# Kernel optimization log

Measured on AMD Instinct MI355X. Metric: run time of the kernel, lower is better.

## Reference

```python
import jax, jax.numpy as jnp
from jax import lax
import numpy as np

EPS = 1e-3  # Keras BatchNormalization default epsilon

def cond_conv(x, experts, rw, rb):
    # x: [B,H,W,Cin]; experts: [E,kh,kw,Cin,Cout]
    pooled = jnp.mean(x, axis=(1, 2))                       # [B,Cin]
    route = jax.nn.sigmoid(pooled @ rw + rb)                # [B,E]
    kernels = jnp.einsum('be,ehwio->bhwio', route, experts) # per-example kernel
    def conv1(xi, ki):
        return lax.conv_general_dilated(
            xi[None], ki, window_strides=(1, 1), padding='SAME',
            dimension_numbers=('NHWC', 'HWIO', 'NHWC'))[0]
    return jax.vmap(conv1)(x, kernels)

def bn_inf(x, gamma, beta, mean, var):
    inv = gamma * lax.rsqrt(var + EPS)
    return x * inv + (beta - mean * inv)

def maxpool2(x):
    return lax.reduce_window(x, -jnp.inf, lax.max,
                             (1, 2, 2, 1), (1, 2, 2, 1), 'SAME')

def se_block(x, w1, w2):
    s = jnp.mean(x, axis=(1, 2))          # [B,C]
    s = jax.nn.relu(s @ w1)
    s = jax.nn.sigmoid(s @ w2)
    return x * s[:, None, None, :]

def setup_inputs() -> dict:
    key = jax.random.key(0)
    ks = jax.random.split(key, 12)
    d = {
        'x': jax.random.normal(ks[0], (64, 128, 128, 6), jnp.float32),
        'experts1': jax.random.normal(ks[1], (3, 3, 3, 6, 32), jnp.float32) * 0.1,
        'route1_w': jax.random.normal(ks[2], (6, 3), jnp.float32) * 0.1,
        'route1_b': jnp.zeros((3,), jnp.float32),
        'bn1_gamma': jnp.ones((32,), jnp.float32), 'bn1_beta': jnp.zeros((32,), jnp.float32),
        'bn1_mean': jnp.zeros((32,), jnp.float32), 'bn1_var': jnp.ones((32,), jnp.float32),
        'se1_w1': jax.random.normal(ks[3], (32, 2), jnp.float32) * 0.1,
        'se1_w2': jax.random.normal(ks[4], (2, 32), jnp.float32) * 0.1,
        'experts2': jax.random.normal(ks[5], (3, 3, 3, 32, 64), jnp.float32) * 0.05,
        'route2_w': jax.random.normal(ks[6], (32, 3), jnp.float32) * 0.1,
        'route2_b': jnp.zeros((3,), jnp.float32),
        'bn2_gamma': jnp.ones((64,), jnp.float32), 'bn2_beta': jnp.zeros((64,), jnp.float32),
        'bn2_mean': jnp.zeros((64,), jnp.float32), 'bn2_var': jnp.ones((64,), jnp.float32),
        'se2_w1': jax.random.normal(ks[7], (64, 4), jnp.float32) * 0.1,
        'se2_w2': jax.random.normal(ks[8], (4, 64), jnp.float32) * 0.1,
        'experts3': jax.random.normal(ks[9], (3, 3, 3, 64, 128), jnp.float32) * 0.05,
        'route3_w': jax.random.normal(ks[10], (64, 3), jnp.float32) * 0.1,
        'route3_b': jnp.zeros((3,), jnp.float32),
        'bn3_gamma': jnp.ones((128,), jnp.float32), 'bn3_beta': jnp.zeros((128,), jnp.float32),
        'bn3_mean': jnp.zeros((128,), jnp.float32), 'bn3_var': jnp.ones((128,), jnp.float32),
    }
    return d

def reference(x, experts1, route1_w, route1_b, bn1_gamma, bn1_beta, bn1_mean, bn1_var,
              se1_w1, se1_w2, experts2, route2_w, route2_b, bn2_gamma, bn2_beta,
              bn2_mean, bn2_var, se2_w1, se2_w2, experts3, route3_w, route3_b,
              bn3_gamma, bn3_beta, bn3_mean, bn3_var):
    h = cond_conv(x, experts1, route1_w, route1_b)
    h = jax.nn.relu(bn_inf(h, bn1_gamma, bn1_beta, bn1_mean, bn1_var))
    h = maxpool2(h)                       # [B,64,64,32]
    h = se_block(h, se1_w1, se1_w2)
    h = cond_conv(h, experts2, route2_w, route2_b)
    h = jax.nn.relu(bn_inf(h, bn2_gamma, bn2_beta, bn2_mean, bn2_var))
    h = maxpool2(h)                       # [B,32,32,64]
    h = se_block(h, se2_w1, se2_w2)
    h = cond_conv(h, experts3, route3_w, route3_b)
    h = bn_inf(h, bn3_gamma, bn3_beta, bn3_mean, bn3_var)
    return jnp.mean(h, axis=(1, 2))       # [B,128]
```

## Files before the change

kernel.cpp:

```cpp
#include <hip/hip_runtime.h>

#define EPSBN 1e-3f

typedef unsigned short ushort_t;
typedef __attribute__((ext_vector_type(8))) short bf8;
typedef __attribute__((ext_vector_type(4))) float f4;

__device__ __forceinline__ float sigmoidf_(float z) {
  return 1.0f / (1.0f + expf(-z));
}

__device__ __forceinline__ ushort_t f2bf(float x) {
  union { float f; unsigned u; } v; v.f = x;
  unsigned r = (v.u + 0x7fffu + ((v.u >> 16) & 1u)) >> 16;
  return (ushort_t)r;
}

__global__ void k_mean_x(const float* __restrict__ x, float* __restrict__ part) {
  const int b = blockIdx.x >> 2;
  const int q = blockIdx.x & 3;
  const int tid = threadIdx.x;
  float acc[6] = {0.f, 0.f, 0.f, 0.f, 0.f, 0.f};
  const float* xb = x + (size_t)b * (128 * 128 * 6);
  for (int i = 0; i < 16; ++i) {
    const int p = q * 4096 + i * 256 + tid;
    const float* px = xb + (size_t)p * 6;
#pragma unroll
    for (int c = 0; c < 6; ++c) acc[c] += px[c];
  }
#pragma unroll
  for (int c = 0; c < 6; ++c)
    for (int off = 32; off > 0; off >>= 1) acc[c] += __shfl_down(acc[c], off, 64);
  __shared__ float red[4][6];
  const int lane = tid & 63, w = tid >> 6;
  if (lane == 0) {
#pragma unroll
    for (int c = 0; c < 6; ++c) red[w][c] = acc[c];
  }
  __syncthreads();
  if (tid < 6) {
    part[blockIdx.x * 6 + tid] = red[0][tid] + red[1][tid] + red[2][tid] + red[3][tid];
  }
}

__global__ void k_buildk1(const float* __restrict__ part,
                          const float* __restrict__ experts1,
                          const float* __restrict__ rw, const float* __restrict__ rb,
                          const float* __restrict__ gamma, const float* __restrict__ var,
                          ushort_t* __restrict__ k1b) {
  const int b = blockIdx.x;
  const int tid = threadIdx.x;
  __shared__ float route[3];
  if (tid < 3) {
    float z = rb[tid];
    for (int c = 0; c < 6; ++c) {
      const float s = part[(b * 4 + 0) * 6 + c] + part[(b * 4 + 1) * 6 + c] +
                      part[(b * 4 + 2) * 6 + c] + part[(b * 4 + 3) * 6 + c];
      z += (s * (1.0f / 16384.0f)) * rw[c * 3 + tid];
    }
    route[tid] = sigmoidf_(z);
  }
  __syncthreads();
  const float r0 = route[0], r1 = route[1], r2 = route[2];
  for (int s = tid; s < 3072; s += 256) {
    const int j = s & 7;
    const int lane = (s >> 3) & 63;
    const int nt = (s >> 9) & 1;
    const int ky = s >> 10;
    const int lx = lane & 15, lg = lane >> 4;
    const int co = nt * 16 + lx;
    float val = 0.f;
    if (lg < 3 && j < 6) {
      const int idx = ((ky * 3 + lg) * 6 + j) * 32 + co;
      const float v = r0 * experts1[idx] + r1 * experts1[1728 + idx] + r2 * experts1[3456 + idx];
      val = v * gamma[co] * rsqrtf(var[co] + EPSBN);
    }
    k1b[(size_t)b * 3072 + s] = f2bf(val);
  }
}

__global__ __launch_bounds__(256)
void k_conv1(const float* __restrict__ x, const ushort_t* __restrict__ k1b,
             const float* __restrict__ gamma, const float* __restrict__ beta,
             const float* __restrict__ bnmean, const float* __restrict__ bnvar,
             ushort_t* __restrict__ p1b, float* __restrict__ part_m1) {
  const int bid = blockIdx.x;
  const int b = bid >> 3;
  const int tyi = (bid >> 1) & 3;
  const int txi = bid & 1;
  __shared__ __align__(16) ushort_t patch[34 * 68 * 8];
  __shared__ float mred[4][32];
  const int tid = threadIdx.x;
  const float* xb = x + (size_t)b * (128 * 128 * 6);

  for (int v = tid; v < 34 * 68; v += 256) {
    const int ry = v / 68, p = v - ry * 68;
    const int gy = tyi * 32 - 1 + ry, gx = txi * 64 - 1 + p;
    uint4 u = make_uint4(0u, 0u, 0u, 0u);
    if (((unsigned)gy < 128u) && ((unsigned)gx < 128u)) {
      const float* s = xb + ((size_t)(gy * 128 + gx)) * 6;
      const float2 a0 = *(const float2*)s;
      const float2 a1 = *(const float2*)(s + 2);
      const float2 a2 = *(const float2*)(s + 4);
      u.x = (unsigned)f2bf(a0.x) | ((unsigned)f2bf(a0.y) << 16);
      u.y = (unsigned)f2bf(a1.x) | ((unsigned)f2bf(a1.y) << 16);
      u.z = (unsigned)f2bf(a2.x) | ((unsigned)f2bf(a2.y) << 16);
      u.w = 0u;
    }
    *(uint4*)(patch + (size_t)v * 8) = u;
  }

  const int w = tid >> 6;
  const int lane = tid & 63;
  const int lx = lane & 15, lg = lane >> 4;

  bf8 Bf[3][2];
#pragma unroll
  for (int ky = 0; ky < 3; ++ky)
#pragma unroll
    for (int nt = 0; nt < 2; ++nt)
      Bf[ky][nt] = *(const bf8*)(k1b + (size_t)b * 3072 + ((size_t)((ky * 2 + nt) * 64 + lane)) * 8);

  const int co0 = lx, co1 = 16 + lx;
  const float inv0 = gamma[co0] * rsqrtf(bnvar[co0] + EPSBN);
  const float bias0 = beta[co0] - bnmean[co0] * inv0;
  const float inv1 = gamma[co1] * rsqrtf(bnvar[co1] + EPSBN);
  const float bias1 = beta[co1] - bnmean[co1] * inv1;

  __syncthreads();

  float msum0 = 0.f, msum1 = 0.f;

#pragma unroll
  for (int rp = 0; rp < 4; ++rp) {
    const int y0 = w * 8 + rp * 2;
    const int prow = tyi * 16 + w * 4 + rp;
#pragma unroll
    for (int xt = 0; xt < 4; ++xt) {
      bf8 Af[4];
#pragma unroll
      for (int ri = 0; ri < 4; ++ri)
        Af[ri] = *(const bf8*)(patch + ((size_t)(y0 + ri) * 68 + xt * 16 + lx + lg) * 8);
      f4 acc0[2], acc1[2];
#pragma unroll
      for (int nt = 0; nt < 2; ++nt) {
        acc0[nt] = (f4){0.f, 0.f, 0.f, 0.f};
        acc1[nt] = (f4){0.f, 0.f, 0.f, 0.f};
      }
#pragma unroll
      for (int ky = 0; ky < 3; ++ky) {
#pragma unroll
        for (int nt = 0; nt < 2; ++nt) {
          acc0[nt] = __builtin_amdgcn_mfma_f32_16x16x32_bf16(Af[ky], Bf[ky][nt], acc0[nt], 0, 0, 0);
          acc1[nt] = __builtin_amdgcn_mfma_f32_16x16x32_bf16(Af[ky + 1], Bf[ky][nt], acc1[nt], 0, 0, 0);
        }
      }
#pragma unroll
      for (int nt = 0; nt < 2; ++nt) {
        const float inv = nt ? inv1 : inv0;
        const float bias = nt ? bias1 : bias0;
        const int co = nt * 16 + lx;
#pragma unroll
        for (int q = 0; q < 2; ++q) {
          const float m0 = fmaxf(acc0[nt][2 * q] + bias, 0.f);
          const float m1 = fmaxf(acc0[nt][2 * q + 1] + bias, 0.f);
          const float m2 = fmaxf(acc1[nt][2 * q] + bias, 0.f);
          const float m3 = fmaxf(acc1[nt][2 * q + 1] + bias, 0.f);
          const float mx = fmaxf(fmaxf(m0, m1), fmaxf(m2, m3));
          if (nt) msum1 += mx; else msum0 += mx;
          const int pcol = txi * 32 + xt * 8 + lg * 2 + q;
          p1b[(((size_t)b * 64 + prow) * 64 + pcol) * 32 + co] = f2bf(mx);
        }
      }
    }
  }

  msum0 += __shfl_xor(msum0, 16, 64);
  msum0 += __shfl_xor(msum0, 32, 64);
  msum1 += __shfl_xor(msum1, 16, 64);
  msum1 += __shfl_xor(msum1, 32, 64);
  if (lg == 0) {
    mred[w][lx] = msum0;
    mred[w][16 + lx] = msum1;
  }
  __syncthreads();
  if (tid < 32) {
    part_m1[(size_t)bid * 32 + tid] =
        mred[0][tid] + mred[1][tid] + mred[2][tid] + mred[3][tid];
  }
}

__global__ void k_buildk2(const float* __restrict__ part_m1,
                          const float* __restrict__ experts2,
                          const float* __restrict__ rw, const float* __restrict__ rb,
                          const float* __restrict__ w1, const float* __restrict__ w2,
                          const float* __restrict__ gamma, const float* __restrict__ var,
                          ushort_t* __restrict__ k2pb) {
  const int b = blockIdx.x, tid = threadIdx.x;
  __shared__ float m1[32], h[2], s1[32], route[3];
  if (tid < 32) {
    float s = 0.f;
#pragma unroll
    for (int k = 0; k < 8; ++k) s += part_m1[(size_t)(b * 8 + k) * 32 + tid];
    m1[tid] = s * (1.0f / 4096.0f);
  }
  __syncthreads();
  if (tid < 2) {
    float z = 0.f;
    for (int c = 0; c < 32; ++c) z += m1[c] * w1[c * 2 + tid];
    h[tid] = fmaxf(z, 0.f);
  }
  __syncthreads();
  if (tid < 32) s1[tid] = sigmoidf_(h[0] * w2[tid] + h[1] * w2[32 + tid]);
  __syncthreads();
  if (tid < 3) {
    float z = rb[tid];
    for (int c = 0; c < 32; ++c) z += m1[c] * s1[c] * rw[c * 3 + tid];
    route[tid] = sigmoidf_(z);
  }
  __syncthreads();
  const float r0 = route[0], r1 = route[1], r2 = route[2];
  for (int t = tid; t < 18432; t += 256) {
    const int co = t & 63;
    const int ci = (t >> 6) & 31;
    const int tap = t >> 11;
    const float inv = gamma[co] * rsqrtf(var[co] + EPSBN);
    const float v = r0 * experts2[t] + r1 * experts2[18432 + t] + r2 * experts2[2 * 18432 + t];
    k2pb[(size_t)b * 18432 + ((size_t)tap * 64 + co) * 32 + ci] = f2bf(v * s1[ci] * inv);
  }
}

__global__ __launch_bounds__(256)
void k_conv2(const ushort_t* __restrict__ p1b, const ushort_t* __restrict__ k2pb,
             const float* __restrict__ gamma, const float* __restrict__ beta,
             const float* __restrict__ bnmean, const float* __restrict__ bnvar,
             float* __restrict__ part_s3) {
  const int bi = blockIdx.x;
  const int b = bi >> 5;
  const int tile = (bi >> 1) & 15;
  const int cog = bi & 1;
  const int ty = tile >> 2, tx = tile & 3;
  __shared__ __align__(16) short smem[24480];
  __shared__ float sred[4][2][16][9];
  short* As = smem;
  short* Bs = smem + 12960;
  const int tid = threadIdx.x;

  const ushort_t* pb = p1b + (size_t)b * 131072;
  for (int v = tid; v < 1296; v += 256) {
    const int cell = v >> 2, part = v & 3;
    const int ly = cell / 18, lx2 = cell - ly * 18;
    const int gy = ty * 16 - 1 + ly, gx = tx * 16 - 1 + lx2;
    uint4 d = make_uint4(0u, 0u, 0u, 0u);
    if (((unsigned)gy < 64u) && ((unsigned)gx < 64u))
      d = *(const uint4*)(pb + (((size_t)gy << 6) + gx) * 32 + part * 8);
    *(uint4*)(As + (ly * 18 + lx2) * 40 + part * 8) = d;
  }
  for (int v = tid; v < 1152; v += 256) {
    const int r = v >> 2, part = v & 3;
    const int t = r >> 5, n = r & 31;
    const uint4 d = *(const uint4*)(k2pb + (size_t)b * 18432 +
                                    ((size_t)(t * 64 + cog * 32 + n)) * 32 + part * 8);
    *(uint4*)(Bs + r * 40 + part * 8) = d;
  }
  __syncthreads();

  const int w = tid >> 6;
  const int lane = tid & 63;
  const int lx = lane & 15, lg = lane >> 4;

  f4 acc[4][2];
#pragma unroll
  for (int mt = 0; mt < 4; ++mt)
#pragma unroll
    for (int nt = 0; nt < 2; ++nt)
      acc[mt][nt] = (f4){0.f, 0.f, 0.f, 0.f};

#pragma unroll
  for (int t = 0; t < 9; ++t) {
    const int ky = t / 3, kx = t - 3 * (t / 3);
    bf8 Bf0 = *(const bf8*)(Bs + ((t << 5) + lx) * 40 + (lg << 3));
    bf8 Bf1 = *(const bf8*)(Bs + ((t << 5) + 16 + lx) * 40 + (lg << 3));
#pragma unroll
    for (int mt = 0; mt < 4; ++mt) {
      const int y = 4 * w + mt + ky;
      const bf8 Af = *(const bf8*)(As + (y * 18 + lx + kx) * 40 + (lg << 3));
      acc[mt][0] = __builtin_amdgcn_mfma_f32_16x16x32_bf16(Af, Bf0, acc[mt][0], 0, 0, 0);
      acc[mt][1] = __builtin_amdgcn_mfma_f32_16x16x32_bf16(Af, Bf1, acc[mt][1], 0, 0, 0);
    }
  }

  float s3[2][9];
#pragma unroll
  for (int nt = 0; nt < 2; ++nt)
#pragma unroll
    for (int t = 0; t < 9; ++t) s3[nt][t] = 0.f;

#pragma unroll
  for (int half = 0; half < 2; ++half) {
    const int prow = ty * 8 + 2 * w + half;
    const bool rok0 = (prow < 31), rok2 = (prow > 0);
#pragma unroll
    for (int q = 0; q < 2; ++q) {
      const int pcol = tx * 8 + 2 * lg + q;
      const bool cok0 = (pcol < 31), cok2 = (pcol > 0);
      const bool rok[3] = {rok0, true, rok2};
      const bool cok[3] = {cok0, true, cok2};
#pragma unroll
      for (int nt = 0; nt < 2; ++nt) {
        const int co = cog * 32 + nt * 16 + lx;
        const float inv = gamma[co] * rsqrtf(bnvar[co] + EPSBN);
        const float bias = beta[co] - bnmean[co] * inv;
        const float m0 = fmaxf(acc[2 * half][nt][2 * q] + bias, 0.f);
        const float m1 = fmaxf(acc[2 * half][nt][2 * q + 1] + bias, 0.f);
        const float m2 = fmaxf(acc[2 * half + 1][nt][2 * q] + bias, 0.f);
        const float m3 = fmaxf(acc[2 * half + 1][nt][2 * q + 1] + bias, 0.f);
        const float mx = fmaxf(fmaxf(m0, m1), fmaxf(m2, m3));
#pragma unroll
        for (int ky = 0; ky < 3; ++ky)
#pragma unroll
          for (int kx = 0; kx < 3; ++kx)
            if (rok[ky] && cok[kx]) s3[nt][ky * 3 + kx] += mx;
      }
    }
  }

#pragma unroll
  for (int nt = 0; nt < 2; ++nt)
#pragma unroll
    for (int t = 0; t < 9; ++t) {
      float v = s3[nt][t];
      v += __shfl_xor(v, 16, 64);
      v += __shfl_xor(v, 32, 64);
      s3[nt][t] = v;
    }
  __syncthreads();
  if (lg == 0) {
#pragma unroll
    for (int nt = 0; nt < 2; ++nt)
#pragma unroll
      for (int t = 0; t < 9; ++t) sred[w][nt][lx][t] = s3[nt][t];
  }
  __syncthreads();
  for (int v = tid; v < 288; v += 256) {
    const int tap = v >> 5;
    const int colocal = v & 31;
    const int nt = colocal >> 4, lxx = colocal & 15;
    part_s3[(size_t)bi * 288 + v] =
        sred[0][nt][lxx][tap] + sred[1][nt][lxx][tap] +
        sred[2][nt][lxx][tap] + sred[3][nt][lxx][tap];
  }
}

__global__ __launch_bounds__(512)
void k_final(const float* __restrict__ part_s3, const float* __restrict__ experts3,
             const float* __restrict__ rw, const float* __restrict__ rb,
             const float* __restrict__ w1, const float* __restrict__ w2,
             const float* __restrict__ gamma, const float* __restrict__ beta,
             const float* __restrict__ bnmean, const float* __restrict__ bnvar,
             float* __restrict__ out) {
  const int b = blockIdx.x;
  const int tid = threadIdx.x;
  __shared__ float S_loc[9][64], Sp[9][64], m2[64], h[4], s2[64], route[3], redf[4][128];

  for (int v = tid; v < 576; v += 512) {
    const int tap = v >> 6, ci = v & 63;
    const int cg = ci >> 5, colocal = ci & 31;
    float s = 0.f;
#pragma unroll
    for (int tile = 0; tile < 16; ++tile)
      s += part_s3[(size_t)((b * 16 + tile) * 2 + cg) * 288 + tap * 32 + colocal];
    S_loc[tap][ci] = s;
  }
  __syncthreads();
  if (tid < 64) m2[tid] = S_loc[4][tid] * (1.0f / 1024.0f);
  __syncthreads();
  if (tid < 4) {
    float z = 0.f;
    for (int c = 0; c < 64; ++c) z += m2[c] * w1[c * 4 + tid];
    h[tid] = fmaxf(z, 0.f);
  }
  __syncthreads();
  if (tid < 64) {
    float z = 0.f;
#pragma unroll
    for (int j = 0; j < 4; ++j) z += h[j] * w2[j * 64 + tid];
    s2[tid] = sigmoidf_(z);
  }
  __syncthreads();
  if (tid < 3) {
    float z = rb[tid];
    for (int c = 0; c < 64; ++c) z += m2[c] * s2[c] * rw[c * 3 + tid];
    route[tid] = sigmoidf_(z);
  }
  __syncthreads();
  for (int v = tid; v < 576; v += 512) {
    const int tap = v >> 6, ci = v & 63;
    Sp[tap][ci] = S_loc[tap][ci] * s2[ci];
  }
  __syncthreads();

  const int co = tid & 127;
  const int quarter = tid >> 7;
  const int tap_lo = (quarter == 0) ? 0 : (2 * quarter + 1);
  const int tap_hi = tap_lo + ((quarter == 0) ? 3 : 2);
  float acc = 0.f;
#pragma unroll
  for (int e = 0; e < 3; ++e) {
    float m = 0.f;
    for (int tap = tap_lo; tap < tap_hi; ++tap) {
      const float* E = experts3 + ((size_t)(e * 9 + tap) * 64) * 128 + co;
#pragma unroll 16
      for (int ci = 0; ci < 64; ++ci) m = fmaf(E[(size_t)ci * 128], Sp[tap][ci], m);
    }
    acc += route[e] * m;
  }
  redf[quarter][co] = acc;
  __syncthreads();
  if (tid < 128) {
    const float total = redf[0][tid] + redf[1][tid] + redf[2][tid] + redf[3][tid];
    const float inv = gamma[tid] * rsqrtf(bnvar[tid] + EPSBN);
    out[(size_t)b * 128 + tid] = total * (1.0f / 1024.0f) * inv + (beta[tid] - bnmean[tid] * inv);
  }
}

extern "C" void kernel_launch(void* const* d_in, const int* in_sizes, int n_in,
                              void* d_out, int out_size, void* d_ws, size_t ws_size,
                              hipStream_t stream) {
  const float* x        = (const float*)d_in[0];
  const float* experts1 = (const float*)d_in[1];
  const float* rw1      = (const float*)d_in[2];
  const float* rb1      = (const float*)d_in[3];
  const float* g1  = (const float*)d_in[4];
  const float* be1 = (const float*)d_in[5];
  const float* mu1 = (const float*)d_in[6];
  const float* va1 = (const float*)d_in[7];
  const float* sw1a = (const float*)d_in[8];
  const float* sw1b = (const float*)d_in[9];
  const float* experts2 = (const float*)d_in[10];
  const float* rw2 = (const float*)d_in[11];
  const float* rb2 = (const float*)d_in[12];
  const float* g2  = (const float*)d_in[13];
  const float* be2 = (const float*)d_in[14];
  const float* mu2 = (const float*)d_in[15];
  const float* va2 = (const float*)d_in[16];
  const float* sw2a = (const float*)d_in[17];
  const float* sw2b = (const float*)d_in[18];
  const float* experts3 = (const float*)d_in[19];
  const float* rw3 = (const float*)d_in[20];
  const float* rb3 = (const float*)d_in[21];
  const float* g3  = (const float*)d_in[22];
  const float* be3 = (const float*)d_in[23];
  const float* mu3 = (const float*)d_in[24];
  const float* va3 = (const float*)d_in[25];
  float* out = (float*)d_out;
  float* ws = (float*)d_ws;

  float* meanx_part = ws;
  float* part_m1    = ws + 1536;
  ushort_t* k1b     = (ushort_t*)(ws + 17920);
  ushort_t* k2pb    = (ushort_t*)(ws + 116224);
  float* part_s3    = ws + 706048;
  ushort_t* p1b     = (ushort_t*)(ws + 1295872);

  hipLaunchKernelGGL(k_mean_x, dim3(256), dim3(256), 0, stream, x, meanx_part);
  hipLaunchKernelGGL(k_buildk1, dim3(64), dim3(256), 0, stream,
                     meanx_part, experts1, rw1, rb1, g1, va1, k1b);
  hipLaunchKernelGGL(k_conv1, dim3(512), dim3(256), 0, stream,
                     x, k1b, g1, be1, mu1, va1, p1b, part_m1);
  hipLaunchKernelGGL(k_buildk2, dim3(64), dim3(256), 0, stream,
                     part_m1, experts2, rw2, rb2, sw1a, sw1b, g2, va2, k2pb);
  hipLaunchKernelGGL(k_conv2, dim3(2048), dim3(256), 0, stream,
                     p1b, k2pb, g2, be2, mu2, va2, part_s3);
  hipLaunchKernelGGL(k_final, dim3(64), dim3(512), 0, stream,
                     part_s3, experts3, rw3, rb3, sw2a, sw2b, g3, be3, mu3, va3, out);
}
```

Before: 207.3 us.

## Fuse conv1 kernel build into conv1, vectorize mean, reuse A fragments, restructure border sums

The k_buildk1 kernel is removed and conv1 now computes the routing and builds its bf16 weight fragments in registers, which saves a launch and a global round trip. k_mean_x switches to float4 contiguous loads. Both conv kernels load A fragments once and reuse them across output rows or taps, which cuts LDS reads. k_buildk2 is spread over three times as many blocks. conv2 now records the total plus border row, column and corner sums, and the final kernel rebuilds the per-tap sums from these by inclusion-exclusion. That reduces the conditional accumulation and hoists the BN constants out of the loop, at the cost of more registers and redundant weight construction in every conv1 block.

```diff
diff --git a/kernel.cpp b/kernel.cpp
--- a/kernel.cpp
+++ b/kernel.cpp
@@ -21,12 +21,17 @@
   const int q = blockIdx.x & 3;
   const int tid = threadIdx.x;
   float acc[6] = {0.f, 0.f, 0.f, 0.f, 0.f, 0.f};
-  const float* xb = x + (size_t)b * (128 * 128 * 6);
-  for (int i = 0; i < 16; ++i) {
-    const int p = q * 4096 + i * 256 + tid;
-    const float* px = xb + (size_t)p * 6;
-#pragma unroll
-    for (int c = 0; c < 6; ++c) acc[c] += px[c];
+  const float* xb = x + (size_t)b * 98304 + (size_t)q * 24576;
+  for (int p = 0; p < 4; ++p) {
+    const float* base = xb + (size_t)p * 6144 + (size_t)tid * 24;
+#pragma unroll
+    for (int k = 0; k < 6; ++k) {
+      const float4 v = *(const float4*)(base + k * 4);
+      acc[(4 * k + 0) % 6] += v.x;
+      acc[(4 * k + 1) % 6] += v.y;
+      acc[(4 * k + 2) % 6] += v.z;
+      acc[(4 * k + 3) % 6] += v.w;
+    }
   }
 #pragma unroll
   for (int c = 0; c < 6; ++c)
@@ -43,44 +48,10 @@
   }
 }
 
-__global__ void k_buildk1(const float* __restrict__ part,
-                          const float* __restrict__ experts1,
-                          const float* __restrict__ rw, const float* __restrict__ rb,
-                          const float* __restrict__ gamma, const float* __restrict__ var,
-                          ushort_t* __restrict__ k1b) {
-  const int b = blockIdx.x;
-  const int tid = threadIdx.x;
-  __shared__ float route[3];
-  if (tid < 3) {
-    float z = rb[tid];
-    for (int c = 0; c < 6; ++c) {
-      const float s = part[(b * 4 + 0) * 6 + c] + part[(b * 4 + 1) * 6 + c] +
-                      part[(b * 4 + 2) * 6 + c] + part[(b * 4 + 3) * 6 + c];
-      z += (s * (1.0f / 16384.0f)) * rw[c * 3 + tid];
-    }
-    route[tid] = sigmoidf_(z);
-  }
-  __syncthreads();
-  const float r0 = route[0], r1 = route[1], r2 = route[2];
-  for (int s = tid; s < 3072; s += 256) {
-    const int j = s & 7;
-    const int lane = (s >> 3) & 63;
-    const int nt = (s >> 9) & 1;
-    const int ky = s >> 10;
-    const int lx = lane & 15, lg = lane >> 4;
-    const int co = nt * 16 + lx;
-    float val = 0.f;
-    if (lg < 3 && j < 6) {
-      const int idx = ((ky * 3 + lg) * 6 + j) * 32 + co;
-      const float v = r0 * experts1[idx] + r1 * experts1[1728 + idx] + r2 * experts1[3456 + idx];
-      val = v * gamma[co] * rsqrtf(var[co] + EPSBN);
-    }
-    k1b[(size_t)b * 3072 + s] = f2bf(val);
-  }
-}
-
 __global__ __launch_bounds__(256)
-void k_conv1(const float* __restrict__ x, const ushort_t* __restrict__ k1b,
+void k_conv1(const float* __restrict__ x, const float* __restrict__ meanx_part,
+             const float* __restrict__ experts1,
+             const float* __restrict__ rw, const float* __restrict__ rbias,
              const float* __restrict__ gamma, const float* __restrict__ beta,
              const float* __restrict__ bnmean, const float* __restrict__ bnvar,
              ushort_t* __restrict__ p1b, float* __restrict__ part_m1) {
@@ -89,9 +60,20 @@
   const int tyi = (bid >> 1) & 3;
   const int txi = bid & 1;
   __shared__ __align__(16) ushort_t patch[34 * 68 * 8];
+  __shared__ float route_s[3];
   __shared__ float mred[4][32];
   const int tid = threadIdx.x;
   const float* xb = x + (size_t)b * (128 * 128 * 6);
+
+  if (tid < 3) {
+    float z = rbias[tid];
+    for (int c = 0; c < 6; ++c) {
+      const float s = meanx_part[(b * 4 + 0) * 6 + c] + meanx_part[(b * 4 + 1) * 6 + c] +
+                      meanx_part[(b * 4 + 2) * 6 + c] + meanx_part[(b * 4 + 3) * 6 + c];
+      z += (s * (1.0f / 16384.0f)) * rw[c * 3 + tid];
+    }
+    route_s[tid] = sigmoidf_(z);
+  }
 
   for (int v = tid; v < 34 * 68; v += 256) {
     const int ry = v / 68, p = v - ry * 68;
@@ -109,38 +91,50 @@
     }
     *(uint4*)(patch + (size_t)v * 8) = u;
   }
+  __syncthreads();
 
   const int w = tid >> 6;
   const int lane = tid & 63;
   const int lx = lane & 15, lg = lane >> 4;
 
-  bf8 Bf[3][2];
-#pragma unroll
-  for (int ky = 0; ky < 3; ++ky)
-#pragma unroll
-    for (int nt = 0; nt < 2; ++nt)
-      Bf[ky][nt] = *(const bf8*)(k1b + (size_t)b * 3072 + ((size_t)((ky * 2 + nt) * 64 + lane)) * 8);
-
+  const float r0 = route_s[0], r1 = route_s[1], r2 = route_s[2];
   const int co0 = lx, co1 = 16 + lx;
   const float inv0 = gamma[co0] * rsqrtf(bnvar[co0] + EPSBN);
   const float bias0 = beta[co0] - bnmean[co0] * inv0;
   const float inv1 = gamma[co1] * rsqrtf(bnvar[co1] + EPSBN);
   const float bias1 = beta[co1] - bnmean[co1] * inv1;
 
-  __syncthreads();
+  bf8 Bf[3][2];
+#pragma unroll
+  for (int ky = 0; ky < 3; ++ky) {
+#pragma unroll
+    for (int nt = 0; nt < 2; ++nt) {
+      const int co = nt * 16 + lx;
+      const float inv = nt ? inv1 : inv0;
+#pragma unroll
+      for (int j = 0; j < 8; ++j) {
+        float val = 0.f;
+        if (j < 6 && lg < 3) {
+          const int idx = ((ky * 3 + lg) * 6 + j) * 32 + co;
+          val = (r0 * experts1[idx] + r1 * experts1[1728 + idx] +
+                 r2 * experts1[3456 + idx]) * inv;
+        }
+        Bf[ky][nt][j] = (short)f2bf(val);
+      }
+    }
+  }
 
   float msum0 = 0.f, msum1 = 0.f;
 
 #pragma unroll
-  for (int rp = 0; rp < 4; ++rp) {
-    const int y0 = w * 8 + rp * 2;
-    const int prow = tyi * 16 + w * 4 + rp;
-#pragma unroll
-    for (int xt = 0; xt < 4; ++xt) {
-      bf8 Af[4];
-#pragma unroll
-      for (int ri = 0; ri < 4; ++ri)
-        Af[ri] = *(const bf8*)(patch + ((size_t)(y0 + ri) * 68 + xt * 16 + lx + lg) * 8);
+  for (int xt = 0; xt < 4; ++xt) {
+    bf8 Af[10];
+#pragma unroll
+    for (int r = 0; r < 10; ++r)
+      Af[r] = *(const bf8*)(patch + ((size_t)(w * 8 + r) * 68 + xt * 16 + lx + lg) * 8);
+#pragma unroll
+    for (int rp = 0; rp < 4; ++rp) {
+      const int prow = tyi * 16 + w * 4 + rp;
       f4 acc0[2], acc1[2];
 #pragma unroll
       for (int nt = 0; nt < 2; ++nt) {
@@ -151,13 +145,12 @@
       for (int ky = 0; ky < 3; ++ky) {
 #pragma unroll
         for (int nt = 0; nt < 2; ++nt) {
-          acc0[nt] = __builtin_amdgcn_mfma_f32_16x16x32_bf16(Af[ky], Bf[ky][nt], acc0[nt], 0, 0, 0);
-          acc1[nt] = __builtin_amdgcn_mfma_f32_16x16x32_bf16(Af[ky + 1], Bf[ky][nt], acc1[nt], 0, 0, 0);
+          acc0[nt] = __builtin_amdgcn_mfma_f32_16x16x32_bf16(Af[rp * 2 + ky], Bf[ky][nt], acc0[nt], 0, 0, 0);
+          acc1[nt] = __builtin_amdgcn_mfma_f32_16x16x32_bf16(Af[rp * 2 + ky + 1], Bf[ky][nt], acc1[nt], 0, 0, 0);
         }
       }
 #pragma unroll
       for (int nt = 0; nt < 2; ++nt) {
-        const float inv = nt ? inv1 : inv0;
         const float bias = nt ? bias1 : bias0;
         const int co = nt * 16 + lx;
 #pragma unroll
@@ -196,7 +189,9 @@
                           const float* __restrict__ w1, const float* __restrict__ w2,
                           const float* __restrict__ gamma, const float* __restrict__ var,
                           ushort_t* __restrict__ k2pb) {
-  const int b = blockIdx.x, tid = threadIdx.x;
+  const int b = blockIdx.x / 3;
+  const int seg = blockIdx.x - b * 3;
+  const int tid = threadIdx.x;
   __shared__ float m1[32], h[2], s1[32], route[3];
   if (tid < 32) {
     float s = 0.f;
@@ -220,7 +215,8 @@
   }
   __syncthreads();
   const float r0 = route[0], r1 = route[1], r2 = route[2];
-  for (int t = tid; t < 18432; t += 256) {
+  const int t_lo = seg * 6144, t_hi = t_lo + 6144;
+  for (int t = t_lo + tid; t < t_hi; t += 256) {
     const int co = t & 63;
     const int ci = (t >> 6) & 31;
     const int tap = t >> 11;
@@ -241,7 +237,6 @@
   const int cog = bi & 1;
   const int ty = tile >> 2, tx = tile & 3;
   __shared__ __align__(16) short smem[24480];
-  __shared__ float sred[4][2][16][9];
   short* As = smem;
   short* Bs = smem + 12960;
   const int tid = threadIdx.x;
@@ -277,50 +272,61 @@
       acc[mt][nt] = (f4){0.f, 0.f, 0.f, 0.f};
 
 #pragma unroll
-  for (int t = 0; t < 9; ++t) {
-    const int ky = t / 3, kx = t - 3 * (t / 3);
-    bf8 Bf0 = *(const bf8*)(Bs + ((t << 5) + lx) * 40 + (lg << 3));
-    bf8 Bf1 = *(const bf8*)(Bs + ((t << 5) + 16 + lx) * 40 + (lg << 3));
-#pragma unroll
-    for (int mt = 0; mt < 4; ++mt) {
-      const int y = 4 * w + mt + ky;
-      const bf8 Af = *(const bf8*)(As + (y * 18 + lx + kx) * 40 + (lg << 3));
-      acc[mt][0] = __builtin_amdgcn_mfma_f32_16x16x32_bf16(Af, Bf0, acc[mt][0], 0, 0, 0);
-      acc[mt][1] = __builtin_amdgcn_mfma_f32_16x16x32_bf16(Af, Bf1, acc[mt][1], 0, 0, 0);
-    }
-  }
-
-  float s3[2][9];
+  for (int kx = 0; kx < 3; ++kx) {
+    bf8 Af[6];
+#pragma unroll
+    for (int r = 0; r < 6; ++r)
+      Af[r] = *(const bf8*)(As + ((4 * w + r) * 18 + lx + kx) * 40 + (lg << 3));
+#pragma unroll
+    for (int ky = 0; ky < 3; ++ky) {
+      const int t = ky * 3 + kx;
+      const bf8 Bf0 = *(const bf8*)(Bs + ((t << 5) + lx) * 40 + (lg << 3));
+      const bf8 Bf1 = *(const bf8*)(Bs + ((t << 5) + 16 + lx) * 40 + (lg << 3));
+#pragma unroll
+      for (int mt = 0; mt < 4; ++mt) {
+        acc[mt][0] = __builtin_amdgcn_mfma_f32_16x16x32_bf16(Af[ky + mt], Bf0, acc[mt][0], 0, 0, 0);
+        acc[mt][1] = __builtin_amdgcn_mfma_f32_16x16x32_bf16(Af[ky + mt], Bf1, acc[mt][1], 0, 0, 0);
+      }
+    }
+  }
+
+  float inv[2], bias[2];
+#pragma unroll
+  for (int nt = 0; nt < 2; ++nt) {
+    const int co = cog * 32 + nt * 16 + lx;
+    inv[nt] = gamma[co] * rsqrtf(bnvar[co] + EPSBN);
+    bias[nt] = beta[co] - bnmean[co] * inv[nt];
+  }
+  float agg[2][9];
 #pragma unroll
   for (int nt = 0; nt < 2; ++nt)
 #pragma unroll
-    for (int t = 0; t < 9; ++t) s3[nt][t] = 0.f;
+    for (int a = 0; a < 9; ++a) agg[nt][a] = 0.f;
 
 #pragma unroll
   for (int half = 0; half < 2; ++half) {
     const int prow = ty * 8 + 2 * w + half;
-    const bool rok0 = (prow < 31), rok2 = (prow > 0);
+    const bool rT = (prow == 0), rB = (prow == 31);
 #pragma unroll
     for (int q = 0; q < 2; ++q) {
       const int pcol = tx * 8 + 2 * lg + q;
-      const bool cok0 = (pcol < 31), cok2 = (pcol > 0);
-      const bool rok[3] = {rok0, true, rok2};
-      const bool cok[3] = {cok0, true, cok2};
+      const bool cL = (pcol == 0), cR = (pcol == 31);
 #pragma unroll
       for (int nt = 0; nt < 2; ++nt) {
-        const int co = cog * 32 + nt * 16 + lx;
-        const float inv = gamma[co] * rsqrtf(bnvar[co] + EPSBN);
-        const float bias = beta[co] - bnmean[co] * inv;
-        const float m0 = fmaxf(acc[2 * half][nt][2 * q] + bias, 0.f);
-        const float m1 = fmaxf(acc[2 * half][nt][2 * q + 1] + bias, 0.f);
-        const float m2 = fmaxf(acc[2 * half + 1][nt][2 * q] + bias, 0.f);
-        const float m3 = fmaxf(acc[2 * half + 1][nt][2 * q + 1] + bias, 0.f);
+        const float m0 = fmaxf(acc[2 * half][nt][2 * q] + bias[nt], 0.f);
+        const float m1 = fmaxf(acc[2 * half][nt][2 * q + 1] + bias[nt], 0.f);
+        const float m2 = fmaxf(acc[2 * half + 1][nt][2 * q] + bias[nt], 0.f);
+        const float m3 = fmaxf(acc[2 * half + 1][nt][2 * q + 1] + bias[nt], 0.f);
         const float mx = fmaxf(fmaxf(m0, m1), fmaxf(m2, m3));
-#pragma unroll
-        for (int ky = 0; ky < 3; ++ky)
-#pragma unroll
-          for (int kx = 0; kx < 3; ++kx)
-            if (rok[ky] && cok[kx]) s3[nt][ky * 3 + kx] += mx;
+        agg[nt][0] += mx;
+        if (rT) agg[nt][1] += mx;
+        if (rB) agg[nt][2] += mx;
+        if (cL) agg[nt][3] += mx;
+        if (cR) agg[nt][4] += mx;
+        if (rT && cL) agg[nt][5] += mx;
+        if (rT && cR) agg[nt][6] += mx;
+        if (rB && cL) agg[nt][7] += mx;
+        if (rB && cR) agg[nt][8] += mx;
       }
     }
   }
@@ -328,27 +334,30 @@
 #pragma unroll
   for (int nt = 0; nt < 2; ++nt)
 #pragma unroll
-    for (int t = 0; t < 9; ++t) {
-      float v = s3[nt][t];
+    for (int a = 0; a < 9; ++a) {
+      float v = agg[nt][a];
       v += __shfl_xor(v, 16, 64);
       v += __shfl_xor(v, 32, 64);
-      s3[nt][t] = v;
-    }
-  __syncthreads();
+      agg[nt][a] = v;
+    }
+  __syncthreads();
+  float* sred = (float*)smem;
   if (lg == 0) {
 #pragma unroll
     for (int nt = 0; nt < 2; ++nt)
 #pragma unroll
-      for (int t = 0; t < 9; ++t) sred[w][nt][lx][t] = s3[nt][t];
+      for (int a = 0; a < 9; ++a)
+        sred[((w * 2 + nt) * 16 + lx) * 9 + a] = agg[nt][a];
   }
   __syncthreads();
   for (int v = tid; v < 288; v += 256) {
-    const int tap = v >> 5;
+    const int a = v >> 5;
     const int colocal = v & 31;
     const int nt = colocal >> 4, lxx = colocal & 15;
-    part_s3[(size_t)bi * 288 + v] =
-        sred[0][nt][lxx][tap] + sred[1][nt][lxx][tap] +
-        sred[2][nt][lxx][tap] + sred[3][nt][lxx][tap];
+    float s = 0.f;
+#pragma unroll
+    for (int ww = 0; ww < 4; ++ww) s += sred[((ww * 2 + nt) * 16 + lxx) * 9 + a];
+    part_s3[(size_t)bi * 288 + v] = s;
   }
 }
 
@@ -361,19 +370,19 @@
              float* __restrict__ out) {
   const int b = blockIdx.x;
   const int tid = threadIdx.x;
-  __shared__ float S_loc[9][64], Sp[9][64], m2[64], h[4], s2[64], route[3], redf[4][128];
+  __shared__ float AG[9][64], Sp[9][64], m2[64], h[4], s2[64], route[3], redf[4][128];
 
   for (int v = tid; v < 576; v += 512) {
-    const int tap = v >> 6, ci = v & 63;
+    const int a = v >> 6, ci = v & 63;
     const int cg = ci >> 5, colocal = ci & 31;
     float s = 0.f;
 #pragma unroll
     for (int tile = 0; tile < 16; ++tile)
-      s += part_s3[(size_t)((b * 16 + tile) * 2 + cg) * 288 + tap * 32 + colocal];
-    S_loc[tap][ci] = s;
-  }
-  __syncthreads();
-  if (tid < 64) m2[tid] = S_loc[4][tid] * (1.0f / 1024.0f);
+      s += part_s3[(size_t)((b * 16 + tile) * 2 + cg) * 288 + a * 32 + colocal];
+    AG[a][ci] = s;
+  }
+  __syncthreads();
+  if (tid < 64) m2[tid] = AG[0][tid] * (1.0f / 1024.0f);
   __syncthreads();
   if (tid < 4) {
     float z = 0.f;
@@ -396,7 +405,16 @@
   __syncthreads();
   for (int v = tid; v < 576; v += 512) {
     const int tap = v >> 6, ci = v & 63;
-    Sp[tap][ci] = S_loc[tap][ci] * s2[ci];
+    const int ky = tap / 3, kx = tap - 3 * ky;
+    const float T = AG[0][ci];
+    const float A = (ky == 0) ? AG[2][ci] : ((ky == 2) ? AG[1][ci] : 0.f);
+    const float B = (kx == 0) ? AG[4][ci] : ((kx == 2) ? AG[3][ci] : 0.f);
+    float AB = 0.f;
+    if (ky == 0 && kx == 0) AB = AG[8][ci];
+    else if (ky == 0 && kx == 2) AB = AG[7][ci];
+    else if (ky == 2 && kx == 0) AB = AG[6][ci];
+    else if (ky == 2 && kx == 2) AB = AG[5][ci];
+    Sp[tap][ci] = (T - A - B + AB) * s2[ci];
   }
   __syncthreads();
 
@@ -458,17 +476,14 @@
 
   float* meanx_part = ws;
   float* part_m1    = ws + 1536;
-  ushort_t* k1b     = (ushort_t*)(ws + 17920);
-  ushort_t* k2pb    = (ushort_t*)(ws + 116224);
-  float* part_s3    = ws + 706048;
-  ushort_t* p1b     = (ushort_t*)(ws + 1295872);
+  ushort_t* k2pb    = (ushort_t*)(ws + 17920);
+  float* part_s3    = ws + 607744;
+  ushort_t* p1b     = (ushort_t*)(ws + 1197568);
 
   hipLaunchKernelGGL(k_mean_x, dim3(256), dim3(256), 0, stream, x, meanx_part);
-  hipLaunchKernelGGL(k_buildk1, dim3(64), dim3(256), 0, stream,
-                     meanx_part, experts1, rw1, rb1, g1, va1, k1b);
   hipLaunchKernelGGL(k_conv1, dim3(512), dim3(256), 0, stream,
-                     x, k1b, g1, be1, mu1, va1, p1b, part_m1);
-  hipLaunchKernelGGL(k_buildk2, dim3(64), dim3(256), 0, stream,
+                     x, meanx_part, experts1, rw1, rb1, g1, be1, mu1, va1, p1b, part_m1);
+  hipLaunchKernelGGL(k_buildk2, dim3(192), dim3(256), 0, stream,
                      part_m1, experts2, rw2, rb2, sw1a, sw1b, g2, va2, k2pb);
   hipLaunchKernelGGL(k_conv2, dim3(2048), dim3(256), 0, stream,
                      p1b, k2pb, g2, be2, mu2, va2, part_s3);
```

New measurement: 187.9 us. 9.4% less time.
